# Performance work log

Measured on AMD Instinct MI355X. Metric: run time of the kernel, lower is better.

The kernel has to match this reference:

```python
import jax, jax.numpy as jnp
import numpy as np

B, L, S, H, E = 2, 2048, 2048, 16, 64


def setup_inputs() -> dict:
    key = jax.random.key(0)
    kq, kk, kv = jax.random.split(key, 3)
    queries = jax.random.normal(kq, (B, L, H, E), dtype=jnp.float32)
    keys = jax.random.normal(kk, (B, S, H, E), dtype=jnp.float32)
    values = jax.random.normal(kv, (B, S, H, E), dtype=jnp.float32)
    attn_mask = jnp.ones((B, 1, L, S), dtype=jnp.float32)  # >0.5 means attend
    return {"queries": queries, "keys": keys, "values": values, "attn_mask": attn_mask}


def reference(queries, keys, values, attn_mask):
    # queries: [B,L,H,E], keys/values: [B,S,H,E], attn_mask broadcastable to [B,H,L,S]
    E_ = queries.shape[-1]
    scale = 1.0 / np.sqrt(E_).astype(np.float32)
    scores = jnp.einsum('blhe,bshe->bhls', queries, keys)  # [B,H,L,S]
    large_negative = jnp.float32(-1e9)
    scores = scores + jnp.where(attn_mask > 0.5, jnp.float32(0.0), large_negative)
    A = jax.nn.softmax(scale * scores, axis=-1)  # dropout p=0.0 -> identity
    V = jnp.einsum('bhls,bshd->bhld', A, values)  # [B,H,L,D]
    return V
```

## Files before the change

### kernel.cpp

```cpp
#include <hip/hip_runtime.h>

typedef float    f32x4 __attribute__((ext_vector_type(4)));
typedef _Float16 f16x2 __attribute__((ext_vector_type(2)));
typedef _Float16 f16x4 __attribute__((ext_vector_type(4)));
typedef _Float16 f16x8 __attribute__((ext_vector_type(8)));
typedef int      i32x4 __attribute__((ext_vector_type(4)));

namespace {
constexpr int B_ = 2, L_ = 2048, S_ = 2048, H_ = 16, E_ = 64;
constexpr int MBLK = 128;
constexpr int NT = 64;
constexpr int NTILES = S_ / NT;

#define SCALE2f 0.1803368801111204f
#define MBIAS2f -1.8033688e8f

constexpr size_t KHOFF = (size_t)1 << 20;
constexpr size_t VHOFF = KHOFF + (size_t)B_ * H_ * S_ * E_ * 2;

__device__ __forceinline__ f16x2 cvt2(float a, float b) {
  return __builtin_bit_cast(f16x2, __builtin_amdgcn_cvt_pkrtz(a, b));
}
__device__ __forceinline__ int pkh(float a, float b) {
  return __builtin_bit_cast(int, __builtin_amdgcn_cvt_pkrtz(a, b));
}
union H8 { f16x8 v; i32x4 i; f16x4 h4[2]; };
union H4 { f16x4 v; f16x2 h[2]; };

#define GLOAD_LDS16(g, l)                                              \
  __builtin_amdgcn_global_load_lds(                                    \
      (const __attribute__((address_space(1))) void*)(g),              \
      (__attribute__((address_space(3))) void*)(l), 16, 0, 0)
}

extern "C" __global__ __launch_bounds__(256)
void prep_kernel(const float* __restrict__ Kg, const float* __restrict__ Vg,
                 const float* __restrict__ Mg, _Float16* __restrict__ Kh,
                 _Float16* __restrict__ Vh, unsigned long long* __restrict__ Wb) {
  __shared__ _Float16 T[64][72];
  const int bid = blockIdx.x;
  const int t   = threadIdx.x;

  if (bid < 2048) {
    const int idx = bid * 256 + t;
    const int j = idx & 7;
    const int h = (idx >> 3) & (H_ - 1);
    const int s = (idx >> 7) & (S_ - 1);
    const int b = idx >> 18;
    const float* src = Kg + ((((size_t)b * S_ + s) * H_ + h) << 6) + j * 8;
    f32x4 x = *(const f32x4*)src, y = *(const f32x4*)(src + 4);
    i32x4 w = {pkh(x[0], x[1]), pkh(x[2], x[3]), pkh(y[0], y[1]), pkh(y[2], y[3])};
    *(i32x4*)(Kh + ((((size_t)b * H_ + h) * S_ + s) << 6) + j * 8) = w;
  } else if (bid < 4096) {
    const int wv2   = t >> 6;
    const int lane2 = t & 63;
    const size_t wave_id = (size_t)(bid - 2048) * 4 + wv2;
    const float* mp = Mg + wave_id * 1024 + lane2 * 4;
    unsigned long long* wp = Wb + wave_id * 16;
#pragma unroll
    for (int k = 0; k < 4; ++k) {
      const f32x4 x = *(const f32x4*)(mp + k * 256);
      const unsigned long long b0 = __ballot(x[0] > 0.5f);
      const unsigned long long b1 = __ballot(x[1] > 0.5f);
      const unsigned long long b2 = __ballot(x[2] > 0.5f);
      const unsigned long long b3 = __ballot(x[3] > 0.5f);
      if (lane2 < 4) {
        const int sh = lane2 * 16;
        const unsigned long long w =
            ((b0 >> sh) & 0xFFFFull) | (((b1 >> sh) & 0xFFFFull) << 16) |
            (((b2 >> sh) & 0xFFFFull) << 32) | (((b3 >> sh) & 0xFFFFull) << 48);
        wp[k * 4 + lane2] = w;
      }
    }
  } else {
    const int vb = bid - 4096;
    const int st = vb & 31;
    const int h  = (vb >> 5) & (H_ - 1);
    const int b  = vb >> 9;
    const int sl = t >> 2;
    const int e0 = (t & 3) << 4;
    const float* src = Vg + ((((size_t)b * S_ + st * 64 + sl) * H_ + h) << 6) + e0;
#pragma unroll
    for (int i = 0; i < 4; ++i) {
      f32x4 x = *(const f32x4*)(src + i * 4);
#pragma unroll
      for (int c = 0; c < 4; ++c) T[e0 + i * 4 + c][sl] = (_Float16)x[c];
    }
    __syncthreads();
    const int er = t >> 2;
    const int s0 = (t & 3) << 4;
    _Float16* dst = Vh + (((((size_t)b * H_ + h) << 6) + er) * S_) + st * 64 + s0;
    *(i32x4*)dst       = *(const i32x4*)&T[er][s0];
    *(i32x4*)(dst + 8) = *(const i32x4*)&T[er][s0 + 8];
  }
}

extern "C" __global__ __launch_bounds__(256, 2)
void fattn_kernel(const float* __restrict__ Qg, const _Float16* __restrict__ Kh,
                  const _Float16* __restrict__ Vh, const unsigned long long* __restrict__ Wb,
                  float* __restrict__ Og) {
  __shared__ __align__(16) _Float16 Ks[3][NT][64];
  __shared__ __align__(16) _Float16 Vt[3][E_][64];

  const int tid  = threadIdx.x;
  const int wv   = tid >> 6;
  const int lane = tid & 63;
  const int qd   = lane >> 4;
  const int cl   = lane & 15;
  const int sw   = cl & 7;

  const int bid = blockIdx.x;
  const int qb  = bid >> 5;
  const int bh  = bid & 31;
  const int h   = bh & (H_ - 1);
  const int b   = bh >> 4;

  const int l0 = qb * MBLK + wv * 32;

  f16x8 qf[2][2];
#pragma unroll
  for (int mt = 0; mt < 2; ++mt) {
    const float* qp = Qg + ((((size_t)b * L_ + (l0 + mt * 16 + cl)) * H_ + h) << 6);
#pragma unroll
    for (int kb = 0; kb < 2; ++kb) {
      const int e0 = qd * 8 + kb * 32;
      f32x4 x = *(const f32x4*)(qp + e0);
      f32x4 y = *(const f32x4*)(qp + e0 + 4);
      x *= SCALE2f;
      y *= SCALE2f;
      H8 u;
      u.i = (i32x4){pkh(x[0], x[1]), pkh(x[2], x[3]), pkh(y[0], y[1]), pkh(y[2], y[3])};
      qf[mt][kb] = u.v;
    }
  }

  const int rl  = lane >> 3;
  const int gsl = lane & 7;
  const int gsw = gsl ^ rl;
  const _Float16* khb = Kh + ((((size_t)b * H_ + h) * S_) << 6);
  const _Float16* vhb = Vh + ((((size_t)b * H_ + h) << 6) * (size_t)S_);

  const unsigned long long* wbp = Wb + (((size_t)b * L_ + (l0 + cl)) << 5);

  auto dma = [&](int buf, int t) {
#pragma unroll
    for (int p = 0; p < 2; ++p) {
      const int r0 = p * 32 + wv * 8;
      const _Float16* ksrc = khb + (((size_t)(t * 64 + r0 + rl)) << 6) + gsw * 8;
      GLOAD_LDS16(ksrc, &Ks[buf][r0][0]);
      const _Float16* vsrc = vhb + (size_t)(r0 + rl) * S_ + t * 64 + gsw * 8;
      GLOAD_LDS16(vsrc, &Vt[buf][r0][0]);
    }
  };

  const f32x4 zero4 = {0.f, 0.f, 0.f, 0.f};
  f32x4 acc[2][4];
#pragma unroll
  for (int mt = 0; mt < 2; ++mt)
#pragma unroll
    for (int et = 0; et < 4; ++et) acc[mt][et] = zero4;
  f32x4 rs4[2] = {zero4, zero4};

  unsigned long long mwcur = wbp[0];
  dma(0, 0);
  asm volatile("" ::: "memory");
  unsigned long long mwnext = wbp[1];
  dma(1, 1);
  asm volatile("" ::: "memory");

  int bc = 0;
  for (int t = 0; t < NTILES; ++t) {
    if (t < NTILES - 1)
      asm volatile("s_waitcnt vmcnt(5)" ::: "memory");
    else
      asm volatile("s_waitcnt vmcnt(0)" ::: "memory");
    __builtin_amdgcn_s_barrier();

    unsigned long long mwnext2 = 0;
    const int bn = (bc == 2) ? 0 : bc + 1;
    if (t + 2 < NTILES) {
      const int b2 = (bn == 2) ? 0 : bn + 1;
      mwnext2 = wbp[t + 2];
      dma(b2, t + 2);
    }
    asm volatile("" ::: "memory");

    f32x4 sc[4][2];
#pragma unroll
    for (int nt = 0; nt < 4; ++nt) {
      const _Float16* krow = &Ks[bc][nt * 16 + cl][0];
      const f16x8 a0 = *(const f16x8*)(krow + ((qd ^ sw) << 3));
      const f16x8 a1 = *(const f16x8*)(krow + (((qd + 4) ^ sw) << 3));
#pragma unroll
      for (int mt = 0; mt < 2; ++mt) {
        f32x4 c = zero4;
        c = __builtin_amdgcn_mfma_f32_16x16x32_f16(a0, qf[mt][0], c, 0, 0, 0);
        c = __builtin_amdgcn_mfma_f32_16x16x32_f16(a1, qf[mt][1], c, 0, 0, 0);
        sc[nt][mt] = c;
      }
    }

    H8 pa8[2][2];
    if (mwcur == ~0ull) {
#pragma unroll
      for (int mt = 0; mt < 2; ++mt)
#pragma unroll
        for (int nt = 0; nt < 4; ++nt) {
          f32x4 p;
#pragma unroll
          for (int r = 0; r < 4; ++r)
            p[r] = __builtin_amdgcn_exp2f(sc[nt][mt][r]);
          rs4[mt] += p;
          H4 u;
          u.h[0] = cvt2(p[0], p[1]);
          u.h[1] = cvt2(p[2], p[3]);
          pa8[mt][nt >> 1].h4[nt & 1] = u.v;
        }
    } else {
      const unsigned lo = (unsigned)mwcur;
      const unsigned hi = (unsigned)(mwcur >> 32);
#pragma unroll
      for (int mt = 0; mt < 2; ++mt)
#pragma unroll
        for (int nt = 0; nt < 4; ++nt) {
          const unsigned m0 = lo >> (4 * nt + qd);
          const unsigned m1 = hi >> (4 * nt + qd);
          f32x4 p;
          p[0] = __builtin_amdgcn_exp2f(sc[nt][mt][0] + ((m0 & 1u)       ? 0.f : MBIAS2f));
          p[1] = __builtin_amdgcn_exp2f(sc[nt][mt][1] + ((m0 & 0x10000u) ? 0.f : MBIAS2f));
          p[2] = __builtin_amdgcn_exp2f(sc[nt][mt][2] + ((m1 & 1u)       ? 0.f : MBIAS2f));
          p[3] = __builtin_amdgcn_exp2f(sc[nt][mt][3] + ((m1 & 0x10000u) ? 0.f : MBIAS2f));
          rs4[mt] += p;
          H4 u;
          u.h[0] = cvt2(p[0], p[1]);
          u.h[1] = cvt2(p[2], p[3]);
          pa8[mt][nt >> 1].h4[nt & 1] = u.v;
        }
    }

#pragma unroll
    for (int ntp = 0; ntp < 2; ++ntp)
#pragma unroll
      for (int et = 0; et < 4; ++et) {
        const _Float16* vrow = &Vt[bc][et * 16 + cl][0];
        H8 bv;
        bv.h4[0] = *(const f16x4*)(vrow + ((((ntp * 4 + (qd >> 1)) ^ sw) << 3) + ((qd & 1) << 2)));
        bv.h4[1] = *(const f16x4*)(vrow + ((((ntp * 4 + 2 + (qd >> 1)) ^ sw) << 3) + ((qd & 1) << 2)));
        acc[0][et] = __builtin_amdgcn_mfma_f32_16x16x32_f16(pa8[0][ntp].v, bv.v, acc[0][et], 0, 0, 0);
        acc[1][et] = __builtin_amdgcn_mfma_f32_16x16x32_f16(pa8[1][ntp].v, bv.v, acc[1][et], 0, 0, 0);
      }

    mwcur = mwnext;
    mwnext = mwnext2;
    bc = bn;
  }

#pragma unroll
  for (int mt = 0; mt < 2; ++mt) {
    float v = rs4[mt][0] + rs4[mt][1] + rs4[mt][2] + rs4[mt][3];
    v += __shfl_xor(v, 16, 64);
    v += __shfl_xor(v, 32, 64);
#pragma unroll
    for (int r = 0; r < 4; ++r) {
      const float invq = 1.0f / __shfl(v, qd * 4 + r, 64);
      const int l = l0 + mt * 16 + qd * 4 + r;
      float* op = Og + ((((size_t)b * H_ + h) * L_ + l) << 6) + cl;
#pragma unroll
      for (int et = 0; et < 4; ++et) op[et * 16] = acc[mt][et][r] * invq;
    }
  }
}

extern "C" void kernel_launch(void* const* d_in, const int* in_sizes, int n_in,
                              void* d_out, int out_size, void* d_ws, size_t ws_size,
                              hipStream_t stream) {
  const float* Q = (const float*)d_in[0];
  const float* K = (const float*)d_in[1];
  const float* V = (const float*)d_in[2];
  const float* M = (const float*)d_in[3];
  float* O = (float*)d_out;
  unsigned long long* Wb = (unsigned long long*)d_ws;
  _Float16* Khp = (_Float16*)((char*)d_ws + KHOFF);
  _Float16* Vhp = (_Float16*)((char*)d_ws + VHOFF);

  hipLaunchKernelGGL(prep_kernel, dim3(5120), dim3(256), 0, stream, K, V, M, Khp, Vhp, Wb);
  hipLaunchKernelGGL(fattn_kernel, dim3(B_ * H_ * (L_ / MBLK)), dim3(256), 0, stream,
                     Q, Khp, Vhp, Wb, O);
}
```

Measured before the change: 159.6 us.

## Process K/V tiles in pairs with four-buffer LDS pipeline

Replaces the triple-buffered per-tile loop with a quad-buffered loop that handles two 64-key tiles per iteration, prefetching two tiles ahead and refilling both buffers after computing. This halves the number of vmcnt waits and barriers per key tile, which is meant to reduce synchronization overhead. In exchange it adds a second barrier before the refill, raises LDS use to 64 KB per block (which may limit occupancy at 2 blocks per CU), and the prefetch is issued only after compute rather than overlapping it.

```diff
diff --git a/kernel.cpp b/kernel.cpp
--- a/kernel.cpp
+++ b/kernel.cpp
@@ -11,6 +11,7 @@
 constexpr int MBLK = 128;
 constexpr int NT = 64;
 constexpr int NTILES = S_ / NT;
+constexpr int NPAIRS = NTILES / 2;
 
 #define SCALE2f 0.1803368801111204f
 #define MBIAS2f -1.8033688e8f
@@ -99,8 +100,8 @@
 void fattn_kernel(const float* __restrict__ Qg, const _Float16* __restrict__ Kh,
                   const _Float16* __restrict__ Vh, const unsigned long long* __restrict__ Wb,
                   float* __restrict__ Og) {
-  __shared__ __align__(16) _Float16 Ks[3][NT][64];
-  __shared__ __align__(16) _Float16 Vt[3][E_][64];
+  __shared__ __align__(16) _Float16 Ks[4][NT][64];
+  __shared__ __align__(16) _Float16 Vt[4][E_][64];
 
   const int tid  = threadIdx.x;
   const int wv   = tid >> 6;
@@ -161,34 +162,12 @@
     for (int et = 0; et < 4; ++et) acc[mt][et] = zero4;
   f32x4 rs4[2] = {zero4, zero4};
 
-  unsigned long long mwcur = wbp[0];
-  dma(0, 0);
-  asm volatile("" ::: "memory");
-  unsigned long long mwnext = wbp[1];
-  dma(1, 1);
-  asm volatile("" ::: "memory");
-
-  int bc = 0;
-  for (int t = 0; t < NTILES; ++t) {
-    if (t < NTILES - 1)
-      asm volatile("s_waitcnt vmcnt(5)" ::: "memory");
-    else
-      asm volatile("s_waitcnt vmcnt(0)" ::: "memory");
-    __builtin_amdgcn_s_barrier();
-
-    unsigned long long mwnext2 = 0;
-    const int bn = (bc == 2) ? 0 : bc + 1;
-    if (t + 2 < NTILES) {
-      const int b2 = (bn == 2) ? 0 : bn + 1;
-      mwnext2 = wbp[t + 2];
-      dma(b2, t + 2);
-    }
-    asm volatile("" ::: "memory");
-
+  auto tilec = [&](int buf, unsigned long long mw) {
     f32x4 sc[4][2];
+    const _Float16* kb0 = &Ks[buf][0][0];
 #pragma unroll
     for (int nt = 0; nt < 4; ++nt) {
-      const _Float16* krow = &Ks[bc][nt * 16 + cl][0];
+      const _Float16* krow = kb0 + (nt * 16 + cl) * 64;
       const f16x8 a0 = *(const f16x8*)(krow + ((qd ^ sw) << 3));
       const f16x8 a1 = *(const f16x8*)(krow + (((qd + 4) ^ sw) << 3));
 #pragma unroll
@@ -201,7 +180,7 @@
     }
 
     H8 pa8[2][2];
-    if (mwcur == ~0ull) {
+    if (mw == ~0ull) {
 #pragma unroll
       for (int mt = 0; mt < 2; ++mt)
 #pragma unroll
@@ -217,8 +196,8 @@
           pa8[mt][nt >> 1].h4[nt & 1] = u.v;
         }
     } else {
-      const unsigned lo = (unsigned)mwcur;
-      const unsigned hi = (unsigned)(mwcur >> 32);
+      const unsigned lo = (unsigned)mw;
+      const unsigned hi = (unsigned)(mw >> 32);
 #pragma unroll
       for (int mt = 0; mt < 2; ++mt)
 #pragma unroll
@@ -238,21 +217,50 @@
         }
     }
 
+    const _Float16* vb0 = &Vt[buf][0][0];
 #pragma unroll
     for (int ntp = 0; ntp < 2; ++ntp)
 #pragma unroll
       for (int et = 0; et < 4; ++et) {
-        const _Float16* vrow = &Vt[bc][et * 16 + cl][0];
+        const _Float16* vrow = vb0 + (et * 16 + cl) * 64;
         H8 bv;
         bv.h4[0] = *(const f16x4*)(vrow + ((((ntp * 4 + (qd >> 1)) ^ sw) << 3) + ((qd & 1) << 2)));
         bv.h4[1] = *(const f16x4*)(vrow + ((((ntp * 4 + 2 + (qd >> 1)) ^ sw) << 3) + ((qd & 1) << 2)));
         acc[0][et] = __builtin_amdgcn_mfma_f32_16x16x32_f16(pa8[0][ntp].v, bv.v, acc[0][et], 0, 0, 0);
         acc[1][et] = __builtin_amdgcn_mfma_f32_16x16x32_f16(pa8[1][ntp].v, bv.v, acc[1][et], 0, 0, 0);
       }
-
-    mwcur = mwnext;
-    mwnext = mwnext2;
-    bc = bn;
+  };
+
+  unsigned long long m0 = wbp[0], m1 = wbp[1];
+  dma(0, 0);
+  dma(1, 1);
+  asm volatile("" ::: "memory");
+  unsigned long long m2 = wbp[2], m3 = wbp[3];
+  dma(2, 2);
+  dma(3, 3);
+  asm volatile("" ::: "memory");
+
+  for (int p = 0; p < NPAIRS; ++p) {
+    if (p < NPAIRS - 1)
+      asm volatile("s_waitcnt vmcnt(10)" ::: "memory");
+    else
+      asm volatile("s_waitcnt vmcnt(0)" ::: "memory");
+    __builtin_amdgcn_s_barrier();
+
+    const int b0 = (p & 1) << 1;
+    tilec(b0, m0);
+    tilec(b0 + 1, m1);
+
+    unsigned long long m4 = 0, m5 = 0;
+    if (p + 2 < NPAIRS) {
+      __builtin_amdgcn_s_barrier();
+      m4 = wbp[2 * p + 4];
+      m5 = wbp[2 * p + 5];
+      dma(b0, 2 * p + 4);
+      dma(b0 + 1, 2 * p + 5);
+      asm volatile("" ::: "memory");
+    }
+    m0 = m2; m1 = m3; m2 = m4; m3 = m5;
   }
 
 #pragma unroll
```

Measured after the change: 158.9 us. Within noise of the previous version (-0.4%).

## Split key tile across wave pairs, each wave covering 64 query rows

Applied to the files above, without the earlier changes.

Each wave now handles 64 query rows instead of 32. Wave pairs split the 64-key tile in half, so a wave computes 32 keys × 64 queries. Each K/V fragment loaded from LDS is reused across four m-tiles, which cuts LDS reads per MFMA. The V transpose in prep is reordered so a single 16-byte LDS read supplies the PV operand. The cost is a final cross-wave reduction of the partial accumulators and row sums through shared memory, plus higher register pressure from the doubled accumulators.

```diff
diff --git a/kernel.cpp b/kernel.cpp
--- a/kernel.cpp
+++ b/kernel.cpp
@@ -88,10 +88,16 @@
     }
     __syncthreads();
     const int er = t >> 2;
-    const int s0 = (t & 3) << 4;
-    _Float16* dst = Vh + (((((size_t)b * H_ + h) << 6) + er) * S_) + st * 64 + s0;
-    *(i32x4*)dst       = *(const i32x4*)&T[er][s0];
-    *(i32x4*)(dst + 8) = *(const i32x4*)&T[er][s0 + 8];
+    const int u  = t & 3;
+    const int C  = ((u >> 1) << 3) + ((u & 1) << 1);
+    _Float16* dst = Vh + (((((size_t)b * H_ + h) << 6) + er) * S_) + st * 64 + u * 16;
+    H8 w;
+    w.h4[0] = *(const f16x4*)&T[er][(C) * 4];
+    w.h4[1] = *(const f16x4*)&T[er][(C + 4) * 4];
+    *(i32x4*)dst = w.i;
+    w.h4[0] = *(const f16x4*)&T[er][(C + 1) * 4];
+    w.h4[1] = *(const f16x4*)&T[er][(C + 5) * 4];
+    *(i32x4*)(dst + 8) = w.i;
   }
 }
 
@@ -105,6 +111,8 @@
   const int tid  = threadIdx.x;
   const int wv   = tid >> 6;
   const int lane = tid & 63;
+  const int h2   = wv & 1;
+  const int wq   = wv >> 1;
   const int qd   = lane >> 4;
   const int cl   = lane & 15;
   const int sw   = cl & 7;
@@ -115,11 +123,11 @@
   const int h   = bh & (H_ - 1);
   const int b   = bh >> 4;
 
-  const int l0 = qb * MBLK + wv * 32;
-
-  f16x8 qf[2][2];
-#pragma unroll
-  for (int mt = 0; mt < 2; ++mt) {
+  const int l0 = qb * MBLK + wq * 64;
+
+  f16x8 qf[4][2];
+#pragma unroll
+  for (int mt = 0; mt < 4; ++mt) {
     const float* qp = Qg + ((((size_t)b * L_ + (l0 + mt * 16 + cl)) * H_ + h) << 6);
 #pragma unroll
     for (int kb = 0; kb < 2; ++kb) {
@@ -154,12 +162,12 @@
   };
 
   const f32x4 zero4 = {0.f, 0.f, 0.f, 0.f};
-  f32x4 acc[2][4];
-#pragma unroll
-  for (int mt = 0; mt < 2; ++mt)
+  f32x4 acc[4][4];
+#pragma unroll
+  for (int mt = 0; mt < 4; ++mt)
 #pragma unroll
     for (int et = 0; et < 4; ++et) acc[mt][et] = zero4;
-  f32x4 rs4[2] = {zero4, zero4};
+  f32x4 rs4[4] = {zero4, zero4, zero4, zero4};
 
   unsigned long long mwcur = wbp[0];
   dma(0, 0);
@@ -185,14 +193,15 @@
     }
     asm volatile("" ::: "memory");
 
-    f32x4 sc[4][2];
-#pragma unroll
-    for (int nt = 0; nt < 4; ++nt) {
-      const _Float16* krow = &Ks[bc][nt * 16 + cl][0];
+    f32x4 sc[2][4];
+    const _Float16* kb0 = &Ks[bc][h2 * 32][0];
+#pragma unroll
+    for (int nt = 0; nt < 2; ++nt) {
+      const _Float16* krow = kb0 + (nt * 16 + cl) * 64;
       const f16x8 a0 = *(const f16x8*)(krow + ((qd ^ sw) << 3));
       const f16x8 a1 = *(const f16x8*)(krow + (((qd + 4) ^ sw) << 3));
 #pragma unroll
-      for (int mt = 0; mt < 2; ++mt) {
+      for (int mt = 0; mt < 4; ++mt) {
         f32x4 c = zero4;
         c = __builtin_amdgcn_mfma_f32_16x16x32_f16(a0, qf[mt][0], c, 0, 0, 0);
         c = __builtin_amdgcn_mfma_f32_16x16x32_f16(a1, qf[mt][1], c, 0, 0, 0);
@@ -200,12 +209,12 @@
       }
     }
 
-    H8 pa8[2][2];
+    H8 pa8[4];
     if (mwcur == ~0ull) {
 #pragma unroll
-      for (int mt = 0; mt < 2; ++mt)
-#pragma unroll
-        for (int nt = 0; nt < 4; ++nt) {
+      for (int mt = 0; mt < 4; ++mt)
+#pragma unroll
+        for (int nt = 0; nt < 2; ++nt) {
           f32x4 p;
 #pragma unroll
           for (int r = 0; r < 4; ++r)
@@ -214,17 +223,18 @@
           H4 u;
           u.h[0] = cvt2(p[0], p[1]);
           u.h[1] = cvt2(p[2], p[3]);
-          pa8[mt][nt >> 1].h4[nt & 1] = u.v;
+          pa8[mt].h4[nt] = u.v;
         }
     } else {
       const unsigned lo = (unsigned)mwcur;
       const unsigned hi = (unsigned)(mwcur >> 32);
 #pragma unroll
-      for (int mt = 0; mt < 2; ++mt)
-#pragma unroll
-        for (int nt = 0; nt < 4; ++nt) {
-          const unsigned m0 = lo >> (4 * nt + qd);
-          const unsigned m1 = hi >> (4 * nt + qd);
+      for (int mt = 0; mt < 4; ++mt)
+#pragma unroll
+        for (int nt = 0; nt < 2; ++nt) {
+          const int ntg = h2 * 2 + nt;
+          const unsigned m0 = lo >> (4 * ntg + qd);
+          const unsigned m1 = hi >> (4 * ntg + qd);
           f32x4 p;
           p[0] = __builtin_amdgcn_exp2f(sc[nt][mt][0] + ((m0 & 1u)       ? 0.f : MBIAS2f));
           p[1] = __builtin_amdgcn_exp2f(sc[nt][mt][1] + ((m0 & 0x10000u) ? 0.f : MBIAS2f));
@@ -234,39 +244,66 @@
           H4 u;
           u.h[0] = cvt2(p[0], p[1]);
           u.h[1] = cvt2(p[2], p[3]);
-          pa8[mt][nt >> 1].h4[nt & 1] = u.v;
+          pa8[mt].h4[nt] = u.v;
         }
     }
 
-#pragma unroll
-    for (int ntp = 0; ntp < 2; ++ntp)
-#pragma unroll
-      for (int et = 0; et < 4; ++et) {
-        const _Float16* vrow = &Vt[bc][et * 16 + cl][0];
-        H8 bv;
-        bv.h4[0] = *(const f16x4*)(vrow + ((((ntp * 4 + (qd >> 1)) ^ sw) << 3) + ((qd & 1) << 2)));
-        bv.h4[1] = *(const f16x4*)(vrow + ((((ntp * 4 + 2 + (qd >> 1)) ^ sw) << 3) + ((qd & 1) << 2)));
-        acc[0][et] = __builtin_amdgcn_mfma_f32_16x16x32_f16(pa8[0][ntp].v, bv.v, acc[0][et], 0, 0, 0);
-        acc[1][et] = __builtin_amdgcn_mfma_f32_16x16x32_f16(pa8[1][ntp].v, bv.v, acc[1][et], 0, 0, 0);
-      }
+    const _Float16* vb0 = &Vt[bc][0][0];
+#pragma unroll
+    for (int et = 0; et < 4; ++et) {
+      const _Float16* vrow = vb0 + (et * 16 + cl) * 64;
+      const f16x8 bv = *(const f16x8*)(vrow + (((h2 * 4 + qd) ^ sw) << 3));
+#pragma unroll
+      for (int mt = 0; mt < 4; ++mt)
+        acc[mt][et] = __builtin_amdgcn_mfma_f32_16x16x32_f16(pa8[mt].v, bv, acc[mt][et], 0, 0, 0);
+    }
 
     mwcur = mwnext;
     mwnext = mwnext2;
     bc = bn;
   }
 
-#pragma unroll
-  for (int mt = 0; mt < 2; ++mt) {
+  float vsum[4];
+#pragma unroll
+  for (int mt = 0; mt < 4; ++mt) {
     float v = rs4[mt][0] + rs4[mt][1] + rs4[mt][2] + rs4[mt][3];
     v += __shfl_xor(v, 16, 64);
     v += __shfl_xor(v, 32, 64);
+    vsum[mt] = v;
+  }
+
+  __syncthreads();
+  f32x4* xscr = (f32x4*)&Ks[0][0][0];
+  float* rscr = (float*)(xscr + 2 * 2 * 4 * 2 * 64);
+#pragma unroll
+  for (int mt = 0; mt < 4; ++mt) {
+    const f32x4 s0 = h2 ? acc[mt][0] : acc[mt][2];
+    const f32x4 s1 = h2 ? acc[mt][1] : acc[mt][3];
+    xscr[(((((wq * 2 + h2) * 4 + mt) * 2) + 0) << 6) + lane] = s0;
+    xscr[(((((wq * 2 + h2) * 4 + mt) * 2) + 1) << 6) + lane] = s1;
+  }
+  if (lane < 16) {
+#pragma unroll
+    for (int mt = 0; mt < 4; ++mt)
+      rscr[((wq * 2 + h2) * 4 + mt) * 16 + cl] = vsum[mt];
+  }
+  __syncthreads();
+
+  const int hp = 1 - h2;
+#pragma unroll
+  for (int mt = 0; mt < 4; ++mt) {
+    const float vtot = vsum[mt] + rscr[((wq * 2 + hp) * 4 + mt) * 16 + cl];
+    f32x4 own0 = h2 ? acc[mt][2] : acc[mt][0];
+    f32x4 own1 = h2 ? acc[mt][3] : acc[mt][1];
+    own0 += xscr[(((((wq * 2 + hp) * 4 + mt) * 2) + 0) << 6) + lane];
+    own1 += xscr[(((((wq * 2 + hp) * 4 + mt) * 2) + 1) << 6) + lane];
 #pragma unroll
     for (int r = 0; r < 4; ++r) {
-      const float invq = 1.0f / __shfl(v, qd * 4 + r, 64);
+      const float invq = 1.0f / __shfl(vtot, qd * 4 + r, 64);
       const int l = l0 + mt * 16 + qd * 4 + r;
       float* op = Og + ((((size_t)b * H_ + h) * L_ + l) << 6) + cl;
-#pragma unroll
-      for (int et = 0; et < 4; ++et) op[et * 16] = acc[mt][et][r] * invq;
+      op[(h2 * 2 + 0) * 16] = own0[r] * invq;
+      op[(h2 * 2 + 1) * 16] = own1[r] * invq;
     }
   }
 }
```

Measured after the change: 173.4 us. +8.7%, slower.
